# Optimization experiments

Hardware: AMD Instinct MI355X
Metric: run time of the kernel (lower is better)

## Reference

```python
import jax, jax.numpy as jnp
import numpy as np

N = 50000       # nodes
E = 800000      # edges (before self-loops)
IN = 64         # in_channels
OUT = 64        # out_channels


def setup_inputs() -> dict:
    key = jax.random.key(0)
    ks = jax.random.split(key, 6)
    X = jax.random.normal(ks[0], (N, IN), jnp.float32)
    H = jax.random.normal(ks[1], (N, OUT), jnp.float32)
    edge_index = jax.random.randint(ks[2], (2, E), 0, N, dtype=jnp.int64)
    edge_weight = jax.random.uniform(ks[3], (E,), jnp.float32)
    fan_in = IN + OUT
    W1 = jax.random.normal(ks[4], (fan_in, 2 * OUT), jnp.float32) / np.sqrt(fan_in).astype(np.float32)
    b1 = jnp.ones((2 * OUT,), jnp.float32)   # TGCN sets graph_conv1.bias to ones
    W2 = jax.random.normal(ks[5], (fan_in, OUT), jnp.float32) / np.sqrt(fan_in).astype(np.float32)
    b2 = jnp.zeros((OUT,), jnp.float32)      # default GCNConv bias init
    return {"X": X, "H": H, "edge_index": edge_index, "edge_weight": edge_weight,
            "W1": W1, "b1": b1, "W2": W2, "b2": b2}


def _gcn_conv(x, W, b, src, dst, w, n):
    """PyG GCNConv: linear transform, add self-loops (fill=1, improved=False),
    symmetric deg^-1/2 normalization, scatter-add aggregation at dst, + bias."""
    x = x @ W                                   # [N, out]
    loop = jnp.arange(n, dtype=src.dtype)
    s = jnp.concatenate([src, loop])            # [E+N]
    d = jnp.concatenate([dst, loop])
    ww = jnp.concatenate([w, jnp.ones((n,), x.dtype)])
    deg = jax.ops.segment_sum(ww, d, num_segments=n)
    dinv = jnp.where(deg > 0, jax.lax.rsqrt(jnp.maximum(deg, 1e-12)), 0.0)
    norm = dinv[s] * ww * dinv[d]               # [E+N]
    msg = x[s] * norm[:, None]                  # gather + scale
    out = jax.ops.segment_sum(msg, d, num_segments=n)  # scatter-add at dst
    return out + b


def reference(X, H, edge_index, edge_weight, W1, b1, W2, b2):
    src, dst = edge_index[0], edge_index[1]
    n = X.shape[0]
    ru = jax.nn.sigmoid(_gcn_conv(jnp.concatenate([X, H], axis=1), W1, b1, src, dst, edge_weight, n))
    r, u = ru[:, :OUT], ru[:, OUT:]             # chunk into reset/update gates
    c = jnp.tanh(_gcn_conv(jnp.concatenate([X, H * r], axis=1), W2, b2, src, dst, edge_weight, n))
    return u * H + (1.0 - u) * c                # new hidden state [N, OUT]
```

## Files before the change

### kernel.cpp

```cpp
#include <hip/hip_runtime.h>
#include <hip/hip_bf16.h>
#include <hip/hip_fp16.h>

#define NN 50000
#define NE 800000
#define NBIN ((NN + 255) / 256)
#define PB ((NE + 1023) / 1024)
#define GB ((NN + 63) / 64)
#define MAXB 4864

typedef __attribute__((ext_vector_type(8))) short bf16x8;
typedef __attribute__((ext_vector_type(4))) float f32x4;

__device__ __forceinline__ unsigned int f2bf(float x) {
    unsigned int u = __float_as_uint(x);
    return (u + 0x7FFFu + ((u >> 16) & 1u)) >> 16;
}
__device__ __forceinline__ float bf2f(unsigned int b) {
    return __uint_as_float(b << 16);
}

__global__ void k_wprep(const float* __restrict__ W1, const float* __restrict__ W2,
                        unsigned short* __restrict__ Wf1,
                        unsigned short* __restrict__ Wf2t,
                        unsigned short* __restrict__ Wf2b) {
    int i = blockIdx.x * 256 + threadIdx.x;
    if (i < 16384) {
        int j = i & 7, l = (i >> 3) & 63, n = (i >> 9) & 7, kc = i >> 12;
        int k = kc * 32 + ((l >> 4) << 3) + j;
        int col = (n << 4) + (l & 15);
        Wf1[i] = (unsigned short)f2bf(W1[k * 128 + col]);
    }
    if (i < 4096) {
        int j = i & 7, l = (i >> 3) & 63, n = (i >> 9) & 3, kc = i >> 11;
        int k = kc * 32 + ((l >> 4) << 3) + j;
        int col = (n << 4) + (l & 15);
        Wf2t[i] = (unsigned short)f2bf(W2[k * 64 + col]);
        Wf2b[i] = (unsigned short)f2bf(W2[(k + 64) * 64 + col]);
    }
}

template <int OUTC, int KC, int SRC, int OMODE>
__device__ __forceinline__ void mgemm_core(
    const float* __restrict__ X, const float* __restrict__ Hm,
    const unsigned int* __restrict__ RUb, const unsigned short* __restrict__ Wf,
    const float* __restrict__ Z2p, const float* __restrict__ dinv,
    unsigned short* __restrict__ outH, float* __restrict__ outF,
    int bid, unsigned short* aS, unsigned short* wS)
{
    constexpr int NT = OUTC / 16;
    const int tid = threadIdx.x;
    const int row0 = bid * 64;

    constexpr int WH = KC * NT * 64 * 8;
    {
        const uint4* Wg4 = reinterpret_cast<const uint4*>(Wf);
        uint4* wS4 = reinterpret_cast<uint4*>(wS);
        #pragma unroll
        for (int i = tid; i < WH / 8; i += 256) wS4[i] = Wg4[i];
    }
    #pragma unroll
    for (int i = tid; i < 64 * KC * 8; i += 256) {
        int row = i / (KC * 8), f4 = i % (KC * 8);
        int g = row0 + row;
        float4 v = {0.f, 0.f, 0.f, 0.f};
        if (g < NN) {
            if (SRC == 0) {
                v = (f4 < 16) ? reinterpret_cast<const float4*>(X)[g * 16 + f4]
                              : reinterpret_cast<const float4*>(Hm)[g * 16 + f4 - 16];
            } else if (SRC == 1) {
                v = reinterpret_cast<const float4*>(X)[g * 16 + f4];
            } else {
                v = reinterpret_cast<const float4*>(Hm)[g * 16 + f4];
                unsigned int r0 = RUb[g * 64 + 2 * f4];
                unsigned int r1 = RUb[g * 64 + 2 * f4 + 1];
                v.x *= bf2f(r0 & 0xFFFFu); v.y *= bf2f(r0 >> 16);
                v.z *= bf2f(r1 & 0xFFFFu); v.w *= bf2f(r1 >> 16);
            }
        }
        int k = f4 * 4;
        int kc = k >> 5, ko = k & 31;
        int l = (row & 15) | ((ko >> 3) << 4);
        int j0 = ko & 7;
        int m = row >> 4;
        uint2 pk;
        pk.x = f2bf(v.x) | (f2bf(v.y) << 16);
        pk.y = f2bf(v.z) | (f2bf(v.w) << 16);
        *reinterpret_cast<uint2*>(aS + (((m * KC + kc) * 64 + l) * 8 + j0)) = pk;
    }
    __syncthreads();

    const int wid = tid >> 6, l = tid & 63;
    f32x4 acc[NT];
    #pragma unroll
    for (int n = 0; n < NT; ++n) acc[n] = {0.f, 0.f, 0.f, 0.f};

    const bf16x8* aF = reinterpret_cast<const bf16x8*>(aS);
    const bf16x8* wF = reinterpret_cast<const bf16x8*>(wS);
    #pragma unroll
    for (int kc = 0; kc < KC; ++kc) {
        bf16x8 a = aF[(wid * KC + kc) * 64 + l];
        #pragma unroll
        for (int n = 0; n < NT; ++n) {
            bf16x8 b = wF[(kc * NT + n) * 64 + l];
            acc[n] = __builtin_amdgcn_mfma_f32_16x16x32_bf16(a, b, acc[n], 0, 0, 0);
        }
    }

    const int rbase = row0 + wid * 16 + ((l >> 4) << 2);
    const int cl = l & 15;
    float dv[4];
    if (OMODE == 2) {
        #pragma unroll
        for (int i = 0; i < 4; ++i) {
            int row = rbase + i;
            dv[i] = (row < NN) ? dinv[row] : 0.f;
        }
    }
    #pragma unroll
    for (int n = 0; n < NT; ++n) {
        #pragma unroll
        for (int i = 0; i < 4; ++i) {
            int row = rbase + i;
            if (row >= NN) continue;
            int col = n * 16 + cl;
            if (OMODE == 0) {
                outH[(size_t)row * OUTC + col] = (unsigned short)f2bf(acc[n][i]);
            } else if (OMODE == 1) {
                outF[(size_t)row * OUTC + col] = acc[n][i];
            } else {
                float a2 = (acc[n][i] + Z2p[(size_t)row * 64 + col]) * dv[i];
                outH[(size_t)row * 64 + col] = (unsigned short)f2bf(a2);
            }
        }
    }
}

__launch_bounds__(256)
__global__ void k_build(const float* __restrict__ X, const float* __restrict__ Hm,
                        const unsigned short* __restrict__ Wf1,
                        const unsigned short* __restrict__ Wf2t,
                        unsigned short* __restrict__ Z1b, float* __restrict__ Z2p,
                        const int* __restrict__ dst, int* __restrict__ HT) {
    __shared__ unsigned short aS[8192];
    __shared__ unsigned short wS[16384];
    const int bid = blockIdx.x;
    const int tid = threadIdx.x;
    if (bid < PB) {
        int* hist = reinterpret_cast<int*>(aS);
        for (int i = tid; i < NBIN; i += 256) hist[i] = 0;
        __syncthreads();
        const int base = bid * 1024 + tid;
        #pragma unroll
        for (int k = 0; k < 4; ++k) {
            int e = base + k * 256;
            if (e < NE) atomicAdd(&hist[dst[e] >> 8], 1);
        }
        __syncthreads();
        for (int i = tid; i < NBIN; i += 256) HT[i * PB + bid] = hist[i];
        return;
    }
    if (bid < PB + GB) {
        mgemm_core<128, 4, 0, 0>(X, Hm, nullptr, Wf1, nullptr, nullptr,
                                 Z1b, nullptr, bid - PB, aS, wS);
        return;
    }
    mgemm_core<64, 2, 1, 1>(X, Hm, nullptr, Wf2t, nullptr, nullptr,
                            nullptr, Z2p, bid - PB - GB, aS, wS);
}

__launch_bounds__(256)
__global__ void k_gemm2b(const float* __restrict__ X, const float* __restrict__ Hm,
                         const unsigned int* __restrict__ RUb,
                         const unsigned short* __restrict__ Wf2b,
                         const float* __restrict__ Z2p, const float* __restrict__ dinv,
                         unsigned short* __restrict__ Z2b) {
    __shared__ unsigned short aS[4096];
    __shared__ unsigned short wS[4096];
    mgemm_core<64, 2, 2, 2>(X, Hm, RUb, Wf2b, Z2p, dinv, Z2b, nullptr,
                            blockIdx.x, aS, wS);
}

__launch_bounds__(256)
__global__ void k_scanA1(const int* __restrict__ HT, int* __restrict__ within,
                         int* __restrict__ binTot) {
    __shared__ int lds[PB];
    __shared__ int sc[256];
    __shared__ int carryS;
    const int b = blockIdx.x, tid = threadIdx.x;
    if (tid == 0) carryS = 0;
    for (int i = tid; i < PB; i += 256) lds[i] = HT[b * PB + i];
    __syncthreads();
    for (int c0 = 0; c0 < PB; c0 += 256) {
        int i = c0 + tid;
        int v = (i < PB) ? lds[i] : 0;
        sc[tid] = v;
        __syncthreads();
        #pragma unroll
        for (int off = 1; off < 256; off <<= 1) {
            int t = (tid >= off) ? sc[tid - off] : 0;
            __syncthreads();
            sc[tid] += t;
            __syncthreads();
        }
        int carry = carryS;
        if (i < PB) lds[i] = carry + sc[tid] - v;
        __syncthreads();
        if (tid == 255) carryS = carry + sc[255];
        __syncthreads();
    }
    for (int i = tid; i < PB; i += 256) within[b * PB + i] = lds[i];
    if (tid == 0) binTot[b] = carryS;
}

__launch_bounds__(256)
__global__ void k_scanA2(const int* __restrict__ binTot, int* __restrict__ binStart) {
    __shared__ int sc[256];
    const int tid = threadIdx.x;
    int v = (tid < NBIN) ? binTot[tid] : 0;
    sc[tid] = v;
    __syncthreads();
    #pragma unroll
    for (int off = 1; off < 256; off <<= 1) {
        int t = (tid >= off) ? sc[tid - off] : 0;
        __syncthreads();
        sc[tid] += t;
        __syncthreads();
    }
    if (tid < NBIN) binStart[tid] = sc[tid] - v;
    if (tid == 0) binStart[NBIN] = NE;
}

__launch_bounds__(256)
__global__ void k_scatterA(const int* __restrict__ src, const int* __restrict__ dst,
                           const float* __restrict__ w, const int* __restrict__ binStart,
                           const int* __restrict__ within, uint2* __restrict__ rec) {
    __shared__ int cur[NBIN];
    const int blk = blockIdx.x, tid = threadIdx.x;
    for (int b = tid; b < NBIN; b += 256) cur[b] = binStart[b] + within[b * PB + blk];
    __syncthreads();
    const int base = blk * 1024 + tid;
    #pragma unroll
    for (int k = 0; k < 4; ++k) {
        int e = base + k * 256;
        if (e < NE) {
            int d = dst[e];
            int pos = atomicAdd(&cur[d >> 8], 1);
            unsigned int hn = __half_as_ushort(__float2half(w[e]));
            uint2 r;
            r.x = (unsigned int)src[e] | (hn << 16);
            r.y = (unsigned int)d;
            rec[pos] = r;
        }
    }
}

__launch_bounds__(256)
__global__ void k_phase2(const uint2* __restrict__ rec, const int* __restrict__ binStart,
                         unsigned int* __restrict__ snP, int* __restrict__ start,
                         float* __restrict__ dinv, uint2* __restrict__ Z1b) {
    __shared__ unsigned int rSn[MAXB];
    __shared__ unsigned char rLo[MAXB];
    __shared__ unsigned int outSn[MAXB];
    __shared__ int cnt[256];
    __shared__ int sc[256];
    __shared__ int lstart[256];
    __shared__ int cur[256];
    __shared__ float dls[256];
    const int b = blockIdx.x, tid = threadIdx.x;
    const int e0 = binStart[b];
    int nE = binStart[b + 1] - e0;
    if (nE > MAXB) nE = MAXB;

    cnt[tid] = 0;
    __syncthreads();
    for (int i = tid; i < nE; i += 256) {
        uint2 r = rec[e0 + i];
        rSn[i] = r.x;
        int lo = r.y & 255;
        rLo[i] = (unsigned char)lo;
        atomicAdd(&cnt[lo], 1);
    }
    __syncthreads();
    sc[tid] = cnt[tid];
    __syncthreads();
    #pragma unroll
    for (int off = 1; off < 256; off <<= 1) {
        int t = (tid >= off) ? sc[tid - off] : 0;
        __syncthreads();
        sc[tid] += t;
        __syncthreads();
    }
    lstart[tid] = sc[tid] - cnt[tid];
    cur[tid] = sc[tid] - cnt[tid];
    __syncthreads();
    const int node = b * 256 + tid;
    if (node <= NN) start[node] = e0 + lstart[tid];
    for (int i = tid; i < nE; i += 256) {
        int p = atomicAdd(&cur[rLo[i]], 1);
        outSn[p] = rSn[i];
    }
    __syncthreads();
    for (int i = tid; i < nE; i += 256) snP[e0 + i] = outSn[i];
    {
        int s0 = lstart[tid], c = cnt[tid];
        float sum = 0.f;
        for (int i = s0; i < s0 + c; ++i)
            sum += __half2float(__ushort_as_half((unsigned short)(outSn[i] >> 16)));
        float dv = rsqrtf(1.0f + sum);
        dls[tid] = dv;
        if (node < NN) dinv[node] = dv;
    }
    __syncthreads();
    const int nLoc = (NN - b * 256 < 256) ? (NN - b * 256) : 256;
    for (int i = tid; i < nLoc * 32; i += 256) {
        int l = i >> 5, j = i & 31;
        size_t g = (size_t)(b * 256 + l) * 32 + j;
        uint2 z = Z1b[g];
        float dv = dls[l];
        float z0 = bf2f(z.x & 0xFFFFu) * dv, z1 = bf2f(z.x >> 16) * dv;
        float z2 = bf2f(z.y & 0xFFFFu) * dv, z3 = bf2f(z.y >> 16) * dv;
        uint2 o;
        o.x = f2bf(z0) | (f2bf(z1) << 16);
        o.y = f2bf(z2) | (f2bf(z3) << 16);
        Z1b[g] = o;
    }
}

template <int OUTC, int MODE>
__launch_bounds__(256)
__global__ void k_gather(const int* __restrict__ start, const unsigned int* __restrict__ snP,
                         const uint2* __restrict__ Zb, const float* __restrict__ dinv,
                         const float* __restrict__ bias, const uint2* __restrict__ RUb2,
                         uint2* __restrict__ outB, const float* __restrict__ Hm,
                         float* __restrict__ out) {
    constexpr int GRP = OUTC / 4;
    constexpr int NPB = 256 / GRP;
    const int node = blockIdx.x * NPB + threadIdx.x / GRP;
    const int l = threadIdx.x % GRP;
    if (node >= NN) return;

    const int e0 = start[node], e1 = start[node + 1];

    uint2 zs = Zb[(size_t)node * GRP + l];
    float4 acc;
    acc.x = bf2f(zs.x & 0xFFFFu);
    acc.y = bf2f(zs.x >> 16);
    acc.z = bf2f(zs.y & 0xFFFFu);
    acc.w = bf2f(zs.y >> 16);

    #define EFMA(Z, NM) \
        acc.x += bf2f((Z).x & 0xFFFFu) * (NM); \
        acc.y += bf2f((Z).x >> 16) * (NM);     \
        acc.z += bf2f((Z).y & 0xFFFFu) * (NM); \
        acc.w += bf2f((Z).y >> 16) * (NM);

    int e = e0;
    for (; e + 8 <= e1; e += 8) {
        unsigned sn0 = snP[e],     sn1 = snP[e + 1], sn2 = snP[e + 2], sn3 = snP[e + 3];
        unsigned sn4 = snP[e + 4], sn5 = snP[e + 5], sn6 = snP[e + 6], sn7 = snP[e + 7];
        uint2 z0 = Zb[(size_t)(sn0 & 0xFFFFu) * GRP + l];
        uint2 z1 = Zb[(size_t)(sn1 & 0xFFFFu) * GRP + l];
        uint2 z2 = Zb[(size_t)(sn2 & 0xFFFFu) * GRP + l];
        uint2 z3 = Zb[(size_t)(sn3 & 0xFFFFu) * GRP + l];
        uint2 z4 = Zb[(size_t)(sn4 & 0xFFFFu) * GRP + l];
        uint2 z5 = Zb[(size_t)(sn5 & 0xFFFFu) * GRP + l];
        uint2 z6 = Zb[(size_t)(sn6 & 0xFFFFu) * GRP + l];
        uint2 z7 = Zb[(size_t)(sn7 & 0xFFFFu) * GRP + l];
        float n0 = __half2float(__ushort_as_half((unsigned short)(sn0 >> 16)));
        float n1 = __half2float(__ushort_as_half((unsigned short)(sn1 >> 16)));
        float n2 = __half2float(__ushort_as_half((unsigned short)(sn2 >> 16)));
        float n3 = __half2float(__ushort_as_half((unsigned short)(sn3 >> 16)));
        float n4 = __half2float(__ushort_as_half((unsigned short)(sn4 >> 16)));
        float n5 = __half2float(__ushort_as_half((unsigned short)(sn5 >> 16)));
        float n6 = __half2float(__ushort_as_half((unsigned short)(sn6 >> 16)));
        float n7 = __half2float(__ushort_as_half((unsigned short)(sn7 >> 16)));
        EFMA(z0, n0) EFMA(z1, n1) EFMA(z2, n2) EFMA(z3, n3)
        EFMA(z4, n4) EFMA(z5, n5) EFMA(z6, n6) EFMA(z7, n7)
    }
    if (e + 4 <= e1) {
        unsigned sn0 = snP[e], sn1 = snP[e + 1], sn2 = snP[e + 2], sn3 = snP[e + 3];
        uint2 z0 = Zb[(size_t)(sn0 & 0xFFFFu) * GRP + l];
        uint2 z1 = Zb[(size_t)(sn1 & 0xFFFFu) * GRP + l];
        uint2 z2 = Zb[(size_t)(sn2 & 0xFFFFu) * GRP + l];
        uint2 z3 = Zb[(size_t)(sn3 & 0xFFFFu) * GRP + l];
        float n0 = __half2float(__ushort_as_half((unsigned short)(sn0 >> 16)));
        float n1 = __half2float(__ushort_as_half((unsigned short)(sn1 >> 16)));
        float n2 = __half2float(__ushort_as_half((unsigned short)(sn2 >> 16)));
        float n3 = __half2float(__ushort_as_half((unsigned short)(sn3 >> 16)));
        EFMA(z0, n0) EFMA(z1, n1) EFMA(z2, n2) EFMA(z3, n3)
        e += 4;
    }
    for (; e < e1; ++e) {
        unsigned sn = snP[e];
        float nm = __half2float(__ushort_as_half((unsigned short)(sn >> 16)));
        uint2 z = Zb[(size_t)(sn & 0xFFFFu) * GRP + l];
        EFMA(z, nm)
    }
    #undef EFMA

    const float dv = dinv[node];
    const int c = l * 4;
    float4 bb = *reinterpret_cast<const float4*>(bias + c);
    acc.x = acc.x * dv + bb.x; acc.y = acc.y * dv + bb.y;
    acc.z = acc.z * dv + bb.z; acc.w = acc.w * dv + bb.w;

    if (MODE == 0) {
        float4 o;
        o.x = 1.f / (1.f + expf(-acc.x));
        o.y = 1.f / (1.f + expf(-acc.y));
        o.z = 1.f / (1.f + expf(-acc.z));
        o.w = 1.f / (1.f + expf(-acc.w));
        uint2 pk;
        pk.x = f2bf(o.x) | (f2bf(o.y) << 16);
        pk.y = f2bf(o.z) | (f2bf(o.w) << 16);
        outB[(size_t)node * 32 + l] = pk;
    } else {
        uint2 uu = RUb2[(size_t)node * 32 + 16 + l];
        float u0 = bf2f(uu.x & 0xFFFFu), u1 = bf2f(uu.x >> 16);
        float u2 = bf2f(uu.y & 0xFFFFu), u3 = bf2f(uu.y >> 16);
        float4 h4 = *reinterpret_cast<const float4*>(Hm + (size_t)node * 64 + c);
        float4 o;
        o.x = u0 * h4.x + (1.f - u0) * tanhf(acc.x);
        o.y = u1 * h4.y + (1.f - u1) * tanhf(acc.y);
        o.z = u2 * h4.z + (1.f - u2) * tanhf(acc.z);
        o.w = u3 * h4.w + (1.f - u3) * tanhf(acc.w);
        *reinterpret_cast<float4*>(out + (size_t)node * 64 + c) = o;
    }
}

extern "C" void kernel_launch(void* const* d_in, const int* in_sizes, int n_in,
                              void* d_out, int out_size, void* d_ws, size_t ws_size,
                              hipStream_t stream) {
    const float* X  = (const float*)d_in[0];
    const float* Hm = (const float*)d_in[1];
    const int*   ei = (const int*)d_in[2];
    const float* w  = (const float*)d_in[3];
    const float* W1 = (const float*)d_in[4];
    const float* b1 = (const float*)d_in[5];
    const float* W2 = (const float*)d_in[6];
    const float* b2 = (const float*)d_in[7];
    float* out = (float*)d_out;

    const int* src = ei;
    const int* dst = ei + NE;

    char* p = (char*)d_ws;
    uint2* rec   = (uint2*)p;  p += sizeof(uint2) * NE;
    uint2* Z1b   = (uint2*)p;  p += sizeof(uint2) * NN * 32;
    uint2* Z2b   = (uint2*)p;  p += sizeof(uint2) * NN * 16;
    uint2* RUb2  = (uint2*)p;  p += sizeof(uint2) * NN * 32;
    float* Z2p   = (float*)p;  p += sizeof(float) * NN * 64;
    float* dinv  = (float*)p;  p += sizeof(float) * NN;
    int*   start = (int*)p;    p += sizeof(int) * (NN + 1);
    int*   binTot   = (int*)p; p += sizeof(int) * NBIN;
    int*   binStart = (int*)p; p += sizeof(int) * (NBIN + 1);
    int*   HT       = (int*)p; p += sizeof(int) * NBIN * PB;
    int*   within   = (int*)p; p += sizeof(int) * NBIN * PB;
    unsigned int* snP = (unsigned int*)p; p += sizeof(unsigned int) * NE;
    unsigned short* Wf1  = (unsigned short*)p; p += sizeof(unsigned short) * 16384;
    unsigned short* Wf2t = (unsigned short*)p; p += sizeof(unsigned short) * 4096;
    unsigned short* Wf2b = (unsigned short*)p; p += sizeof(unsigned short) * 4096;

    k_wprep<<<64, 256, 0, stream>>>(W1, W2, Wf1, Wf2t, Wf2b);

    k_build<<<PB + 2 * GB, 256, 0, stream>>>(X, Hm, Wf1, Wf2t,
                                             (unsigned short*)Z1b, Z2p, dst, HT);

    k_scanA1<<<NBIN, 256, 0, stream>>>(HT, within, binTot);
    k_scanA2<<<1, 256, 0, stream>>>(binTot, binStart);
    k_scatterA<<<PB, 256, 0, stream>>>(src, dst, w, binStart, within, rec);
    k_phase2<<<NBIN, 256, 0, stream>>>(rec, binStart, snP, start, dinv, Z1b);

    k_gather<128, 0><<<(NN * 32 + 255) / 256, 256, 0, stream>>>(
        start, snP, Z1b, dinv, b1, nullptr, RUb2, nullptr, nullptr);

    k_gemm2b<<<GB, 256, 0, stream>>>(X, Hm, (const unsigned int*)RUb2, Wf2b,
                                     Z2p, dinv, (unsigned short*)Z2b);
    k_gather<64, 1><<<(NN * 16 + 255) / 256, 256, 0, stream>>>(
        start, snP, Z2b, dinv, b2, RUb2, nullptr, Hm, out);
}
```

Before: 127.0 us.

## Store first-layer features in FP8 for gather and fold bin scan into consumers

The first GCN layer's pre-scaled features are now written as FP8 (e4m3) into a separate buffer, and a dedicated gather kernel reads 4 bytes per lane instead of 8, with an 8-way unrolled edge loop. This halves the bytes moved in the dominant random-gather stage. The single-block bin-prefix scan kernel is removed, and each consumer block recomputes the small scan redundantly in shared memory, saving one launch. FP8 quantisation of the features introduces extra rounding error that may push results toward the tolerance limit.

```diff
diff --git a/kernel.cpp b/kernel.cpp
--- a/kernel.cpp
+++ b/kernel.cpp
@@ -11,6 +11,7 @@
 
 typedef __attribute__((ext_vector_type(8))) short bf16x8;
 typedef __attribute__((ext_vector_type(4))) float f32x4;
+typedef __attribute__((ext_vector_type(2))) float f32x2;
 
 __device__ __forceinline__ unsigned int f2bf(float x) {
     unsigned int u = __float_as_uint(x);
@@ -18,6 +19,18 @@
 }
 __device__ __forceinline__ float bf2f(unsigned int b) {
     return __uint_as_float(b << 16);
+}
+__device__ __forceinline__ float4 f8x4_dec(unsigned int u) {
+    f32x2 lo = __builtin_amdgcn_cvt_pk_f32_fp8(u, false);
+    f32x2 hi = __builtin_amdgcn_cvt_pk_f32_fp8(u, true);
+    float4 r; r.x = lo[0]; r.y = lo[1]; r.z = hi[0]; r.w = hi[1];
+    return r;
+}
+__device__ __forceinline__ unsigned int f8x4_enc(float a, float b, float c, float d) {
+    int q = 0;
+    q = __builtin_amdgcn_cvt_pk_fp8_f32(a, b, q, false);
+    q = __builtin_amdgcn_cvt_pk_fp8_f32(c, d, q, true);
+    return (unsigned int)q;
 }
 
 __global__ void k_wprep(const float* __restrict__ W1, const float* __restrict__ W2,
@@ -214,30 +227,23 @@
 }
 
 __launch_bounds__(256)
-__global__ void k_scanA2(const int* __restrict__ binTot, int* __restrict__ binStart) {
-    __shared__ int sc[256];
-    const int tid = threadIdx.x;
-    int v = (tid < NBIN) ? binTot[tid] : 0;
-    sc[tid] = v;
-    __syncthreads();
-    #pragma unroll
-    for (int off = 1; off < 256; off <<= 1) {
-        int t = (tid >= off) ? sc[tid - off] : 0;
-        __syncthreads();
-        sc[tid] += t;
-        __syncthreads();
-    }
-    if (tid < NBIN) binStart[tid] = sc[tid] - v;
-    if (tid == 0) binStart[NBIN] = NE;
-}
-
-__launch_bounds__(256)
 __global__ void k_scatterA(const int* __restrict__ src, const int* __restrict__ dst,
-                           const float* __restrict__ w, const int* __restrict__ binStart,
+                           const float* __restrict__ w, const int* __restrict__ binTot,
                            const int* __restrict__ within, uint2* __restrict__ rec) {
+    __shared__ int bS[256];
     __shared__ int cur[NBIN];
     const int blk = blockIdx.x, tid = threadIdx.x;
-    for (int b = tid; b < NBIN; b += 256) cur[b] = binStart[b] + within[b * PB + blk];
+    int bv = (tid < NBIN) ? binTot[tid] : 0;
+    bS[tid] = bv;
+    __syncthreads();
+    #pragma unroll
+    for (int off = 1; off < 256; off <<= 1) {
+        int t = (tid >= off) ? bS[tid - off] : 0;
+        __syncthreads();
+        bS[tid] += t;
+        __syncthreads();
+    }
+    if (tid < NBIN) cur[tid] = (bS[tid] - bv) + within[tid * PB + blk];
     __syncthreads();
     const int base = blk * 1024 + tid;
     #pragma unroll
@@ -256,9 +262,10 @@
 }
 
 __launch_bounds__(256)
-__global__ void k_phase2(const uint2* __restrict__ rec, const int* __restrict__ binStart,
+__global__ void k_phase2(const uint2* __restrict__ rec, const int* __restrict__ binTot,
                          unsigned int* __restrict__ snP, int* __restrict__ start,
-                         float* __restrict__ dinv, uint2* __restrict__ Z1b) {
+                         float* __restrict__ dinv, const uint2* __restrict__ Z1b,
+                         unsigned int* __restrict__ Zf8) {
     __shared__ unsigned int rSn[MAXB];
     __shared__ unsigned char rLo[MAXB];
     __shared__ unsigned int outSn[MAXB];
@@ -268,8 +275,20 @@
     __shared__ int cur[256];
     __shared__ float dls[256];
     const int b = blockIdx.x, tid = threadIdx.x;
-    const int e0 = binStart[b];
-    int nE = binStart[b + 1] - e0;
+
+    int bv = (tid < NBIN) ? binTot[tid] : 0;
+    sc[tid] = bv;
+    __syncthreads();
+    #pragma unroll
+    for (int off = 1; off < 256; off <<= 1) {
+        int t = (tid >= off) ? sc[tid - off] : 0;
+        __syncthreads();
+        sc[tid] += t;
+        __syncthreads();
+    }
+    const int e0 = (b == 0) ? 0 : sc[b - 1];
+    int nE = sc[b] - e0;
+    __syncthreads();
     if (nE > MAXB) nE = MAXB;
 
     cnt[tid] = 0;
@@ -318,25 +337,94 @@
         size_t g = (size_t)(b * 256 + l) * 32 + j;
         uint2 z = Z1b[g];
         float dv = dls[l];
-        float z0 = bf2f(z.x & 0xFFFFu) * dv, z1 = bf2f(z.x >> 16) * dv;
-        float z2 = bf2f(z.y & 0xFFFFu) * dv, z3 = bf2f(z.y >> 16) * dv;
-        uint2 o;
-        o.x = f2bf(z0) | (f2bf(z1) << 16);
-        o.y = f2bf(z2) | (f2bf(z3) << 16);
-        Z1b[g] = o;
-    }
-}
-
-template <int OUTC, int MODE>
-__launch_bounds__(256)
-__global__ void k_gather(const int* __restrict__ start, const unsigned int* __restrict__ snP,
-                         const uint2* __restrict__ Zb, const float* __restrict__ dinv,
-                         const float* __restrict__ bias, const uint2* __restrict__ RUb2,
-                         uint2* __restrict__ outB, const float* __restrict__ Hm,
-                         float* __restrict__ out) {
-    constexpr int GRP = OUTC / 4;
-    constexpr int NPB = 256 / GRP;
-    const int node = blockIdx.x * NPB + threadIdx.x / GRP;
+        Zf8[g] = f8x4_enc(bf2f(z.x & 0xFFFFu) * dv, bf2f(z.x >> 16) * dv,
+                          bf2f(z.y & 0xFFFFu) * dv, bf2f(z.y >> 16) * dv);
+    }
+}
+
+__launch_bounds__(256)
+__global__ void k_gather1(const int* __restrict__ start, const unsigned int* __restrict__ snP,
+                          const unsigned int* __restrict__ Zf8, const float* __restrict__ dinv,
+                          const float* __restrict__ bias, uint2* __restrict__ RUb2) {
+    const int node = blockIdx.x * 8 + (threadIdx.x >> 5);
+    const int l = threadIdx.x & 31;
+    if (node >= NN) return;
+
+    const int e0 = start[node], e1 = start[node + 1];
+    float4 acc = f8x4_dec(Zf8[(size_t)node * 32 + l]);
+
+    #define EFMA8(U, NM) { float4 zz = f8x4_dec(U); \
+        acc.x += zz.x * (NM); acc.y += zz.y * (NM); \
+        acc.z += zz.z * (NM); acc.w += zz.w * (NM); }
+
+    int e = e0;
+    for (; e + 8 <= e1; e += 8) {
+        unsigned sn0 = snP[e],     sn1 = snP[e + 1], sn2 = snP[e + 2], sn3 = snP[e + 3];
+        unsigned sn4 = snP[e + 4], sn5 = snP[e + 5], sn6 = snP[e + 6], sn7 = snP[e + 7];
+        unsigned z0 = Zf8[(size_t)(sn0 & 0xFFFFu) * 32 + l];
+        unsigned z1 = Zf8[(size_t)(sn1 & 0xFFFFu) * 32 + l];
+        unsigned z2 = Zf8[(size_t)(sn2 & 0xFFFFu) * 32 + l];
+        unsigned z3 = Zf8[(size_t)(sn3 & 0xFFFFu) * 32 + l];
+        unsigned z4 = Zf8[(size_t)(sn4 & 0xFFFFu) * 32 + l];
+        unsigned z5 = Zf8[(size_t)(sn5 & 0xFFFFu) * 32 + l];
+        unsigned z6 = Zf8[(size_t)(sn6 & 0xFFFFu) * 32 + l];
+        unsigned z7 = Zf8[(size_t)(sn7 & 0xFFFFu) * 32 + l];
+        float n0 = __half2float(__ushort_as_half((unsigned short)(sn0 >> 16)));
+        float n1 = __half2float(__ushort_as_half((unsigned short)(sn1 >> 16)));
+        float n2 = __half2float(__ushort_as_half((unsigned short)(sn2 >> 16)));
+        float n3 = __half2float(__ushort_as_half((unsigned short)(sn3 >> 16)));
+        float n4 = __half2float(__ushort_as_half((unsigned short)(sn4 >> 16)));
+        float n5 = __half2float(__ushort_as_half((unsigned short)(sn5 >> 16)));
+        float n6 = __half2float(__ushort_as_half((unsigned short)(sn6 >> 16)));
+        float n7 = __half2float(__ushort_as_half((unsigned short)(sn7 >> 16)));
+        EFMA8(z0, n0) EFMA8(z1, n1) EFMA8(z2, n2) EFMA8(z3, n3)
+        EFMA8(z4, n4) EFMA8(z5, n5) EFMA8(z6, n6) EFMA8(z7, n7)
+    }
+    if (e + 4 <= e1) {
+        unsigned sn0 = snP[e], sn1 = snP[e + 1], sn2 = snP[e + 2], sn3 = snP[e + 3];
+        unsigned z0 = Zf8[(size_t)(sn0 & 0xFFFFu) * 32 + l];
+        unsigned z1 = Zf8[(size_t)(sn1 & 0xFFFFu) * 32 + l];
+        unsigned z2 = Zf8[(size_t)(sn2 & 0xFFFFu) * 32 + l];
+        unsigned z3 = Zf8[(size_t)(sn3 & 0xFFFFu) * 32 + l];
+        float n0 = __half2float(__ushort_as_half((unsigned short)(sn0 >> 16)));
+        float n1 = __half2float(__ushort_as_half((unsigned short)(sn1 >> 16)));
+        float n2 = __half2float(__ushort_as_half((unsigned short)(sn2 >> 16)));
+        float n3 = __half2float(__ushort_as_half((unsigned short)(sn3 >> 16)));
+        EFMA8(z0, n0) EFMA8(z1, n1) EFMA8(z2, n2) EFMA8(z3, n3)
+        e += 4;
+    }
+    for (; e < e1; ++e) {
+        unsigned sn = snP[e];
+        float nm = __half2float(__ushort_as_half((unsigned short)(sn >> 16)));
+        unsigned z = Zf8[(size_t)(sn & 0xFFFFu) * 32 + l];
+        EFMA8(z, nm)
+    }
+    #undef EFMA8
+
+    const float dv = dinv[node];
+    const int c = l * 4;
+    float4 bb = *reinterpret_cast<const float4*>(bias + c);
+    acc.x = acc.x * dv + bb.x; acc.y = acc.y * dv + bb.y;
+    acc.z = acc.z * dv + bb.z; acc.w = acc.w * dv + bb.w;
+
+    float4 o;
+    o.x = 1.f / (1.f + expf(-acc.x));
+    o.y = 1.f / (1.f + expf(-acc.y));
+    o.z = 1.f / (1.f + expf(-acc.z));
+    o.w = 1.f / (1.f + expf(-acc.w));
+    uint2 pk;
+    pk.x = f2bf(o.x) | (f2bf(o.y) << 16);
+    pk.y = f2bf(o.z) | (f2bf(o.w) << 16);
+    RUb2[(size_t)node * 32 + l] = pk;
+}
+
+__launch_bounds__(256)
+__global__ void k_gather2(const int* __restrict__ start, const unsigned int* __restrict__ snP,
+                          const uint2* __restrict__ Zb, const float* __restrict__ dinv,
+                          const float* __restrict__ bias, const uint2* __restrict__ RUb2,
+                          const float* __restrict__ Hm, float* __restrict__ out) {
+    constexpr int GRP = 16;
+    const int node = blockIdx.x * 16 + threadIdx.x / GRP;
     const int l = threadIdx.x % GRP;
     if (node >= NN) return;
 
@@ -405,28 +493,16 @@
     acc.x = acc.x * dv + bb.x; acc.y = acc.y * dv + bb.y;
     acc.z = acc.z * dv + bb.z; acc.w = acc.w * dv + bb.w;
 
-    if (MODE == 0) {
-        float4 o;
-        o.x = 1.f / (1.f + expf(-acc.x));
-        o.y = 1.f / (1.f + expf(-acc.y));
-        o.z = 1.f / (1.f + expf(-acc.z));
-        o.w = 1.f / (1.f + expf(-acc.w));
-        uint2 pk;
-        pk.x = f2bf(o.x) | (f2bf(o.y) << 16);
-        pk.y = f2bf(o.z) | (f2bf(o.w) << 16);
-        outB[(size_t)node * 32 + l] = pk;
-    } else {
-        uint2 uu = RUb2[(size_t)node * 32 + 16 + l];
-        float u0 = bf2f(uu.x & 0xFFFFu), u1 = bf2f(uu.x >> 16);
-        float u2 = bf2f(uu.y & 0xFFFFu), u3 = bf2f(uu.y >> 16);
-        float4 h4 = *reinterpret_cast<const float4*>(Hm + (size_t)node * 64 + c);
-        float4 o;
-        o.x = u0 * h4.x + (1.f - u0) * tanhf(acc.x);
-        o.y = u1 * h4.y + (1.f - u1) * tanhf(acc.y);
-        o.z = u2 * h4.z + (1.f - u2) * tanhf(acc.z);
-        o.w = u3 * h4.w + (1.f - u3) * tanhf(acc.w);
-        *reinterpret_cast<float4*>(out + (size_t)node * 64 + c) = o;
-    }
+    uint2 uu = RUb2[(size_t)node * 32 + 16 + l];
+    float u0 = bf2f(uu.x & 0xFFFFu), u1 = bf2f(uu.x >> 16);
+    float u2 = bf2f(uu.y & 0xFFFFu), u3 = bf2f(uu.y >> 16);
+    float4 h4 = *reinterpret_cast<const float4*>(Hm + (size_t)node * 64 + c);
+    float4 o;
+    o.x = u0 * h4.x + (1.f - u0) * tanhf(acc.x);
+    o.y = u1 * h4.y + (1.f - u1) * tanhf(acc.y);
+    o.z = u2 * h4.z + (1.f - u2) * tanhf(acc.z);
+    o.w = u3 * h4.w + (1.f - u3) * tanhf(acc.w);
+    *reinterpret_cast<float4*>(out + (size_t)node * 64 + c) = o;
 }
 
 extern "C" void kernel_launch(void* const* d_in, const int* in_sizes, int n_in,
@@ -453,11 +529,11 @@
     float* Z2p   = (float*)p;  p += sizeof(float) * NN * 64;
     float* dinv  = (float*)p;  p += sizeof(float) * NN;
     int*   start = (int*)p;    p += sizeof(int) * (NN + 1);
-    int*   binTot   = (int*)p; p += sizeof(int) * NBIN;
-    int*   binStart = (int*)p; p += sizeof(int) * (NBIN + 1);
+    int*   binTot   = (int*)p; p += sizeof(int) * (NBIN + 1);
     int*   HT       = (int*)p; p += sizeof(int) * NBIN * PB;
     int*   within   = (int*)p; p += sizeof(int) * NBIN * PB;
     unsigned int* snP = (unsigned int*)p; p += sizeof(unsigned int) * NE;
+    unsigned int* Zf8 = (unsigned int*)p; p += sizeof(unsigned int) * NN * 32;
     unsigned short* Wf1  = (unsigned short*)p; p += sizeof(unsigned short) * 16384;
     unsigned short* Wf2t = (unsigned short*)p; p += sizeof(unsigned short) * 4096;
     unsigned short* Wf2b = (unsigned short*)p; p += sizeof(unsigned short) * 4096;
@@ -468,15 +544,12 @@
                                              (unsigned short*)Z1b, Z2p, dst, HT);
 
     k_scanA1<<<NBIN, 256, 0, stream>>>(HT, within, binTot);
-    k_scanA2<<<1, 256, 0, stream>>>(binTot, binStart);
-    k_scatterA<<<PB, 256, 0, stream>>>(src, dst, w, binStart, within, rec);
-    k_phase2<<<NBIN, 256, 0, stream>>>(rec, binStart, snP, start, dinv, Z1b);
-
-    k_gather<128, 0><<<(NN * 32 + 255) / 256, 256, 0, stream>>>(
-        start, snP, Z1b, dinv, b1, nullptr, RUb2, nullptr, nullptr);
+    k_scatterA<<<PB, 256, 0, stream>>>(src, dst, w, binTot, within, rec);
+    k_phase2<<<NBIN, 256, 0, stream>>>(rec, binTot, snP, start, dinv, Z1b, Zf8);
+
+    k_gather1<<<(NN + 7) / 8, 256, 0, stream>>>(start, snP, Zf8, dinv, b1, RUb2);
 
     k_gemm2b<<<GB, 256, 0, stream>>>(X, Hm, (const unsigned int*)RUb2, Wf2b,
                                      Z2p, dinv, (unsigned short*)Z2b);
-    k_gather<64, 1><<<(NN * 16 + 255) / 256, 256, 0, stream>>>(
-        start, snP, Z2b, dinv, b2, RUb2, nullptr, Hm, out);
-}
+    k_gather2<<<(NN + 15) / 16, 256, 0, stream>>>(start, snP, Z2b, dinv, b2, RUb2, Hm, out);
+}
```

Measured after the change: 122.4 us. -3.6%, faster.
